# Performance work log

Hardware: AMD Instinct MI355X
Metric: run time of the kernel (lower is better)

The kernel has to match this reference:

```python
import jax, jax.numpy as jnp
import numpy as np

DIM = 128
N = 4096


def setup_inputs() -> dict:
    key = jax.random.key(0)
    ks = jax.random.split(key, 12)
    d = DIM
    s = 0.02
    inp = jax.random.normal(ks[0], (N, 2 * d), dtype=jnp.float32)
    # H = myLinear: (2d -> 5d -> 1), tanh after each layer
    Hw1 = jax.random.normal(ks[1], (2 * d, 5 * d), dtype=jnp.float32) * s
    Hb1 = jax.random.normal(ks[2], (5 * d,), dtype=jnp.float32) * s
    Hw2 = jax.random.normal(ks[3], (5 * d, 1), dtype=jnp.float32) * s
    Hb2 = jax.random.normal(ks[4], (1,), dtype=jnp.float32) * s
    # augment_f: (d -> 4d -> 8d -> d*d), tanh after each layer
    Aw1 = jax.random.normal(ks[5], (d, 4 * d), dtype=jnp.float32) * s
    Ab1 = jax.random.normal(ks[6], (4 * d,), dtype=jnp.float32) * s
    Aw2 = jax.random.normal(ks[7], (4 * d, 8 * d), dtype=jnp.float32) * s
    Ab2 = jax.random.normal(ks[8], (8 * d,), dtype=jnp.float32) * s
    Aw3 = jax.random.normal(ks[9], (8 * d, d * d), dtype=jnp.float32) * s
    Ab3 = jax.random.normal(ks[10], (d * d,), dtype=jnp.float32) * s
    u = jax.random.uniform(ks[11], (d,), dtype=jnp.float32, minval=-0.001, maxval=0.001)
    return {"t": 0, "inp": inp, "Hw1": Hw1, "Hb1": Hb1, "Hw2": Hw2, "Hb2": Hb2,
            "Aw1": Aw1, "Ab1": Ab1, "Aw2": Aw2, "Ab2": Ab2, "Aw3": Aw3, "Ab3": Ab3, "u": u}


def reference(t, inp, Hw1, Hb1, Hw2, Hb2, Aw1, Ab1, Aw2, Ab2, Aw3, Ab3, u):
    d = DIM
    n = inp.shape[0]

    def H_scalar(z):  # z: [2d] -> scalar
        h = jnp.tanh(z @ Hw1 + Hb1)
        return jnp.tanh(h @ Hw2 + Hb2)[0]

    # per-sample gradient of scalar H w.r.t. input (== batch_jacobian squeeze)
    g = jax.vmap(jax.grad(H_scalar))(inp)  # [N, 2d]
    dx = g[:, :d]
    dv = -g[:, d:]

    x = inp[:, :d]
    h1 = jnp.tanh(x @ Aw1 + Ab1)            # [N, 4d]
    h2 = jnp.tanh(h1 @ Aw2 + Ab2)           # [N, 8d]
    gq = jnp.tanh(h2 @ Aw3 + Ab3).reshape(n, d, d)  # [N, d, d]
    dv = dv + jnp.einsum("nij,j->ni", gq, u)
    return jnp.concatenate([dx, dv], axis=-1)  # [N, 2d]
```

## Files before the change

kernel.cpp:

```cpp
#include <hip/hip_runtime.h>
#include <hip/hip_bf16.h>
#include <cstdint>


typedef __bf16 bf16_t;
typedef __bf16 bf16x4_t __attribute__((ext_vector_type(4)));
typedef __bf16 bf16x8_t __attribute__((ext_vector_type(8)));
typedef float f32x4_t __attribute__((ext_vector_type(4)));
typedef float f32x16_t __attribute__((ext_vector_type(16)));
typedef int intx4_t __attribute__((ext_vector_type(4)));
typedef int intx8_t __attribute__((ext_vector_type(8)));

#define DIMD 128
#define NROW 4096
#define SMEM_G64 8192
#define SMEM3_BYTES 73728

__device__ __forceinline__ float fast_tanh(float x) {
  float t = __builtin_amdgcn_exp2f(x * 2.8853900817779268f);
  return 1.f - 2.f * __builtin_amdgcn_rcpf(t + 1.f);
}

__device__ __forceinline__ uint8_t to_fp8(float x) {
  return (uint8_t)(__builtin_amdgcn_cvt_pk_fp8_f32(x, x, 0, false) & 0xff);
}

__device__ __forceinline__ void g2l16(const void* gp, void* lp) {
  __builtin_amdgcn_global_load_lds(
      reinterpret_cast<__attribute__((address_space(1))) void*>(
          reinterpret_cast<uintptr_t>(gp)),
      reinterpret_cast<__attribute__((address_space(3))) void*>(
          reinterpret_cast<uintptr_t>(lp)),
      16, 0, 0);
}

template <int CTRL>
__device__ __forceinline__ float dpp_addf(float v) {
  return v + __int_as_float(__builtin_amdgcn_update_dpp(
                 0, __float_as_int(v), CTRL, 0xf, 0xf, true));
}
__device__ __forceinline__ float dpp_sum32(float v) {
  v = dpp_addf<0x111>(v);
  v = dpp_addf<0x112>(v);
  v = dpp_addf<0x114>(v);
  v = dpp_addf<0x118>(v);
  v = dpp_addf<0x142>(v);
  return v;
}

template <int EPI>
__device__ __forceinline__ void gemm64_body(char* smem, int bx, int by,
                                            const bf16_t* A, int lda,
                                            const bf16_t* B, int ldb, int K,
                                            const float* bias, void* outp,
                                            int ldo) {
  constexpr int BK = 32;
  bf16_t* As = (bf16_t*)smem;
  bf16_t* Bs = As + 2048;

  const int m0 = bx * 64;
  const int n0 = by * 64;
  const int tid = threadIdx.x;
  const int wave = tid >> 6;
  const int lane = tid & 63;
  const int wm = wave >> 1;
  const int wn = wave & 1;

  const int sr = lane >> 2;
  const int sk = (((lane & 3) ^ ((sr >> 1) & 3)) * 8);
  const int fr = lane & 15;
  const int fk = (((lane >> 4) ^ ((fr >> 1) & 3)) * 8);

  f32x4_t acc[2][2] = {};

  for (int k0 = 0; k0 < K; k0 += BK) {
    if (k0) __syncthreads();
    const int rb = wave * 16;
    g2l16(A + (size_t)(m0 + rb + sr) * lda + (k0 + sk), As + rb * BK);
    g2l16(B + (size_t)(n0 + rb + sr) * ldb + (k0 + sk), Bs + rb * BK);
    __syncthreads();

    bf16x8_t af[2], bb[2];
#pragma unroll
    for (int t = 0; t < 2; ++t) {
      af[t] = *(const bf16x8_t*)(As + (wm * 32 + t * 16 + fr) * BK + fk);
      bb[t] = *(const bf16x8_t*)(Bs + (wn * 32 + t * 16 + fr) * BK + fk);
    }
#pragma unroll
    for (int i = 0; i < 2; ++i)
#pragma unroll
      for (int j = 0; j < 2; ++j)
        acc[i][j] = __builtin_amdgcn_mfma_f32_16x16x32_bf16(af[i], bb[j],
                                                            acc[i][j], 0, 0, 0);
  }

#pragma unroll
  for (int i = 0; i < 2; ++i) {
    const int row = m0 + wm * 32 + i * 16 + (lane >> 4) * 4;
#pragma unroll
    for (int j = 0; j < 2; ++j) {
      const int col = n0 + wn * 32 + j * 16 + fr;
      if constexpr (EPI == 0) {
        bf16_t* O = (bf16_t*)outp;
        const float b = bias[col];
#pragma unroll
        for (int r = 0; r < 4; ++r)
          O[(size_t)(row + r) * ldo + col] = (bf16_t)fast_tanh(acc[i][j][r] + b);
      } else {
        uint8_t* O = (uint8_t*)outp;
        const float b = bias[col];
#pragma unroll
        for (int r = 0; r < 4; ++r)
          O[(size_t)(row + r) * ldo + col] =
              to_fp8(64.f * fast_tanh(acc[i][j][r] + b));
      }
    }
  }
}

__device__ __forceinline__ void hbwd64_body(char* smem, int bx, int by,
                                            const bf16_t* A, int lda,
                                            const bf16_t* B, int ldb, int K,
                                            float* out, int ldo) {
  constexpr int BK = 32;
  bf16_t* As = (bf16_t*)smem;
  bf16_t* Bs = As + 2048;

  const int m0 = bx * 64;
  const int n0 = by * 64;
  const int tid = threadIdx.x;
  const int wave = tid >> 6;
  const int lane = tid & 63;
  const int wm = wave >> 2;
  const int wn = wave & 3;

  const int sr = lane >> 2;
  const int sk = (((lane & 3) ^ ((sr >> 1) & 3)) * 8);
  const int fr = lane & 15;
  const int fk = (((lane >> 4) ^ ((fr >> 1) & 3)) * 8);

  f32x4_t acc[2] = {};

  for (int k0 = 0; k0 < K; k0 += BK) {
    if (k0) __syncthreads();
    if (wave < 4) {
      const int rb = wave * 16;
      g2l16(A + (size_t)(m0 + rb + sr) * lda + (k0 + sk), As + rb * BK);
    } else {
      const int rb = (wave - 4) * 16;
      g2l16(B + (size_t)(n0 + rb + sr) * ldb + (k0 + sk), Bs + rb * BK);
    }
    __syncthreads();

    const bf16x8_t bb = *(const bf16x8_t*)(Bs + (wn * 16 + fr) * BK + fk);
#pragma unroll
    for (int t = 0; t < 2; ++t) {
      const bf16x8_t af =
          *(const bf16x8_t*)(As + (wm * 32 + t * 16 + fr) * BK + fk);
      acc[t] = __builtin_amdgcn_mfma_f32_16x16x32_bf16(af, bb, acc[t], 0, 0, 0);
    }
  }

  const bool dx = (n0 < DIMD);
  const int col = n0 + wn * 16 + fr;
#pragma unroll
  for (int t = 0; t < 2; ++t) {
    const int row = m0 + wm * 32 + t * 16 + (lane >> 4) * 4;
#pragma unroll
    for (int r = 0; r < 4; ++r) {
      const size_t idx = (size_t)(row + r) * ldo + col;
      if (dx) out[idx] = acc[t][r];
      else atomicAdd(&out[idx], -acc[t][r]);
    }
  }
}

__device__ __forceinline__ void a3_body(char* smem, int bx, int by,
                                        const uint8_t* A, const uint8_t* B,
                                        float* out, const float* ab3,
                                        const float* uvec) {
  constexpr int BK = 64, K = 1024, NT = K / BK;
  uint8_t* As = (uint8_t*)smem;
  uint8_t* Bs = As + 49152;

  const int m0 = bx * 256;
  const int n0 = by * 128;
  const int tid = threadIdx.x;
  const int wave = tid >> 6;
  const int lane = tid & 63;
  const int wm = wave >> 1;
  const int wn = wave & 1;

  const int sr = lane >> 2;
  const int sk = ((lane & 3) ^ ((sr >> 1) & 3)) * 16;

  const int rl = lane & 31;
  const int w = (rl >> 1) & 3;
  const int c0 = lane >> 5;
  const int sLo = ((2 * c0) ^ w) * 16;
  const int sHi = ((2 * c0 + 1) ^ w) * 16;

  f32x16_t acc[2][2] = {};

#define A3_STAGE(buf, k0)                                                     \
  do {                                                                        \
    uint8_t* Ad = As + (buf) * 16384;                                         \
    uint8_t* Bd = Bs + (buf) * 8192;                                          \
    _Pragma("unroll") for (int t_ = 0; t_ < 2; ++t_) {                        \
      const int rb_ = wave * 32 + t_ * 16;                                    \
      g2l16(A + (size_t)(m0 + rb_ + sr) * K + ((k0) + sk), Ad + rb_ * BK);    \
    }                                                                         \
    const int rbB_ = wave * 16;                                               \
    g2l16(B + (size_t)(n0 + rbB_ + sr) * K + ((k0) + sk), Bd + rbB_ * BK);    \
  } while (0)

  A3_STAGE(0, 0);
  A3_STAGE(1, BK);
  asm volatile("s_waitcnt vmcnt(3)" ::: "memory");
  __builtin_amdgcn_s_barrier();
  asm volatile("" ::: "memory");

  int cur = 0, pre = 2;
#pragma unroll 1
  for (int t = 0; t < NT; ++t) {
    if (t + 2 < NT) A3_STAGE(pre, (t + 2) * BK);
    const uint8_t* Ab = As + cur * 16384;
    const uint8_t* Bb = Bs + cur * 8192;

    __builtin_amdgcn_s_setprio(1);
    intx8_t bfr[2];
#pragma unroll
    for (int j = 0; j < 2; ++j) {
      const int rb2 = (wn * 64 + j * 32 + rl) * BK;
      intx4_t lob = *(const intx4_t*)(Bb + rb2 + sLo);
      intx4_t hib = *(const intx4_t*)(Bb + rb2 + sHi);
      bfr[j] = __builtin_shufflevector(lob, hib, 0, 1, 2, 3, 4, 5, 6, 7);
    }
#pragma unroll
    for (int i = 0; i < 2; ++i) {
      const int ra = (wm * 64 + i * 32 + rl) * BK;
      intx4_t lo = *(const intx4_t*)(Ab + ra + sLo);
      intx4_t hi = *(const intx4_t*)(Ab + ra + sHi);
      intx8_t af = __builtin_shufflevector(lo, hi, 0, 1, 2, 3, 4, 5, 6, 7);
#pragma unroll
      for (int j = 0; j < 2; ++j)
        acc[i][j] = __builtin_amdgcn_mfma_scale_f32_32x32x64_f8f6f4(
            af, bfr[j], acc[i][j], 0, 0, 0, 0x79797979, 0, 0x79797979);
    }
    __builtin_amdgcn_s_setprio(0);

    if (t < NT - 1) {
      if (t + 2 < NT)
        asm volatile("s_waitcnt vmcnt(3)" ::: "memory");
      else
        asm volatile("s_waitcnt vmcnt(0)" ::: "memory");
      __builtin_amdgcn_s_barrier();
      asm volatile("" ::: "memory");
    }
    cur = (cur == 2) ? 0 : cur + 1;
    pre = (pre == 2) ? 0 : pre + 1;
  }
#undef A3_STAGE

  const int q = lane >> 5;
  const int cA = wn * 64 + rl;
  const float uu0 = uvec[cA];
  const float uu1 = uvec[cA + 32];
  const float b30 = ab3[n0 + cA];
  const float b31 = ab3[n0 + cA + 32];
#pragma unroll
  for (int i = 0; i < 2; ++i) {
    float s16[16];
#pragma unroll
    for (int r = 0; r < 16; ++r)
      s16[r] = fast_tanh(acc[i][0][r] + b30) * uu0 +
               fast_tanh(acc[i][1][r] + b31) * uu1;
#pragma unroll
    for (int r = 0; r < 16; ++r) s16[r] = dpp_sum32(s16[r]);
    if (rl == 31) {
      const int rowb = m0 + wm * 64 + i * 32 + 4 * q;
#pragma unroll
      for (int r = 0; r < 16; ++r)
        atomicAdd(
            &out[(size_t)(rowb + (r & 3) + 8 * (r >> 2)) * 256 + 128 + by],
            s16[r]);
    }
  }
}

__device__ __forceinline__ void tcvt_body(char* smem, const float* in,
                                          bf16_t* out, int R, int C, int bx,
                                          int by) {
  float(*t)[33] = (float(*)[33])smem;
  const int c0 = bx * 32;
  const int r0 = by * 32;
  const int tx = threadIdx.x & 31;
  const int ty = threadIdx.x >> 5;
#pragma unroll
  for (int k = 0; k < 4; ++k)
    t[ty + k * 8][tx] = in[(size_t)(r0 + ty + k * 8) * C + c0 + tx];
  __syncthreads();
#pragma unroll
  for (int k = 0; k < 4; ++k)
    out[(size_t)(c0 + ty + k * 8) * R + r0 + tx] = (bf16_t)t[tx][ty + k * 8];
}

__device__ __forceinline__ void aw3t_body(char* smem, const float* Aw3,
                                          uint8_t* Aw3T8, int b) {
  float(*t)[33] = (float(*)[33])smem;
  const int c0 = (b & 511) * 32;
  const int r0 = (b >> 9) * 32;
  const int tx = threadIdx.x & 31;
  const int ty = threadIdx.x >> 5;
#pragma unroll
  for (int k = 0; k < 4; ++k)
    t[ty + k * 8][tx] = Aw3[(size_t)(r0 + ty + k * 8) * 16384 + c0 + tx];
  __syncthreads();
  const int cl = threadIdx.x >> 3;
  const int j = (threadIdx.x & 7) * 4;
  uchar4 v;
  v.x = to_fp8(64.f * t[j + 0][cl]);
  v.y = to_fp8(64.f * t[j + 1][cl]);
  v.z = to_fp8(64.f * t[j + 2][cl]);
  v.w = to_fp8(64.f * t[j + 3][cl]);
  *(uchar4*)(Aw3T8 + (size_t)(c0 + cl) * 1024 + r0 + j) = v;
}

__device__ __forceinline__ void hgrad_row(int row, const bf16_t* h,
                                          const float* Hw2, const float* Hb2,
                                          bf16_t* wout) {
  const int lane = threadIdx.x & 63;
  float hv[10], wv[10];
  float pre2 = 0.f;
#pragma unroll
  for (int t = 0; t < 10; ++t) {
    const int j = lane + t * 64;
    hv[t] = (float)h[(size_t)row * 640 + j];
    wv[t] = Hw2[j];
    pre2 += hv[t] * wv[t];
  }
#pragma unroll
  for (int d = 1; d < 64; d <<= 1) pre2 += __shfl_xor(pre2, d, 64);
  const float y = fast_tanh(pre2 + Hb2[0]);
  const float s = 1.f - y * y;
#pragma unroll
  for (int t = 0; t < 10; ++t) {
    const int j = lane + t * 64;
    wout[(size_t)row * 640 + j] = (bf16_t)(s * wv[t] * (1.f - hv[t] * hv[t]));
  }
}

__global__ __launch_bounds__(256) void launch0(
    const float* __restrict__ inp, bf16_t* __restrict__ inp_bf,
    const float* __restrict__ Hw1, bf16_t* __restrict__ Hw1T,
    bf16_t* __restrict__ Hw1_bf, const float* __restrict__ Aw1,
    bf16_t* __restrict__ Aw1T, const float* __restrict__ Aw2,
    bf16_t* __restrict__ Aw2T, float* __restrict__ out) {
  __shared__ __align__(16) char smem[4224];
  int b = blockIdx.x;
  if (b < 1024) {
    const int i = b * 256 + threadIdx.x;
    const float4 v = ((const float4*)inp)[i];
    bf16x4_t o = {(bf16_t)v.x, (bf16_t)v.y, (bf16_t)v.z, (bf16_t)v.w};
    ((bf16x4_t*)inp_bf)[i] = o;
  } else if (b < 1184) {
    int s = b - 1024;
    tcvt_body(smem, Hw1, Hw1T, 256, 640, s % 20, s / 20);
  } else if (b < 1248) {
    int s = b - 1184;
    tcvt_body(smem, Aw1, Aw1T, 128, 512, s % 16, s / 16);
  } else if (b < 1760) {
    int s = b - 1248;
    tcvt_body(smem, Aw2, Aw2T, 512, 1024, s % 32, s / 32);
  } else if (b < 1920) {
    const int i = (b - 1760) * 256 + threadIdx.x;
    const float4 v = ((const float4*)Hw1)[i];
    bf16x4_t o = {(bf16_t)v.x, (bf16_t)v.y, (bf16_t)v.z, (bf16_t)v.w};
    ((bf16x4_t*)Hw1_bf)[i] = o;
  } else {
    const int i = (b - 1920) * 256 + threadIdx.x;
    ((float4*)out)[i] = make_float4(0.f, 0.f, 0.f, 0.f);
  }
}

__global__ __launch_bounds__(256) void launch1(
    const bf16_t* __restrict__ inp_bf, const bf16_t* __restrict__ Hw1T,
    const float* __restrict__ Hb1, bf16_t* __restrict__ h_bf,
    const bf16_t* __restrict__ Aw1T, const float* __restrict__ Ab1,
    bf16_t* __restrict__ h1_bf, const float* __restrict__ Aw3,
    uint8_t* __restrict__ Aw3T8) {
  __shared__ __align__(16) char smem[SMEM_G64];
  const int b = blockIdx.x;
  if (b < 640) {
    gemm64_body<0>(smem, b % 64, b / 64, inp_bf, 256, Hw1T, 256, 256, Hb1,
                   h_bf, 640);
  } else if (b < 1152) {
    const int i = b - 640;
    gemm64_body<0>(smem, i % 64, i / 64, inp_bf, 256, Aw1T, 128, 128, Ab1,
                   h1_bf, 512);
  } else {
    aw3t_body(smem, Aw3, Aw3T8, b - 1152);
  }
}

__global__ __launch_bounds__(256) void launch2(
    const bf16_t* __restrict__ h1_bf, const bf16_t* __restrict__ Aw2T,
    const float* __restrict__ Ab2, uint8_t* __restrict__ h2_f8,
    const bf16_t* __restrict__ h_bf, const float* __restrict__ Hw2,
    const float* __restrict__ Hb2, bf16_t* __restrict__ w_bf,
    const float* __restrict__ Aw3, uint8_t* __restrict__ Aw3T8) {
  __shared__ __align__(16) char smem[SMEM_G64];
  const int b = blockIdx.x;
  if (b < 1024) {
    gemm64_body<3>(smem, b % 64, b / 64, h1_bf, 512, Aw2T, 512, 512, Ab2,
                   h2_f8, 1024);
  } else if (b < 2048) {
    const int row = (b - 1024) * 4 + (threadIdx.x >> 6);
    hgrad_row(row, h_bf, Hw2, Hb2, w_bf);
  } else {
    aw3t_body(smem, Aw3, Aw3T8, 8192 + (b - 2048));
  }
}

__global__ __launch_bounds__(512, 4) void launch3(
    const bf16_t* __restrict__ w_bf, const bf16_t* __restrict__ Hw1_bf,
    float* __restrict__ out, const uint8_t* __restrict__ h2_f8,
    const uint8_t* __restrict__ Aw3T8, const float* __restrict__ Ab3,
    const float* __restrict__ uvec) {
  __shared__ __align__(16) char smem[SMEM3_BYTES];
  const int b = blockIdx.x;
  if (b < 256) {
    hbwd64_body(smem, b % 64, b / 64, w_bf, 640, Hw1_bf, 640, 640, out, 256);
  } else {
    const int p = b - 256;
    const int by = (p & 7) * 16 + ((p >> 3) & 15);
    const int bx = p >> 7;
    a3_body(smem, bx, by, h2_f8, Aw3T8, out, Ab3, uvec);
  }
}

extern "C" void kernel_launch(void* const* d_in, const int* in_sizes, int n_in,
                              void* d_out, int out_size, void* d_ws,
                              size_t ws_size, hipStream_t stream) {
  (void)in_sizes; (void)n_in; (void)out_size; (void)ws_size;
  const float* inp = (const float*)d_in[1];
  const float* Hw1 = (const float*)d_in[2];
  const float* Hb1 = (const float*)d_in[3];
  const float* Hw2 = (const float*)d_in[4];
  const float* Hb2 = (const float*)d_in[5];
  const float* Aw1 = (const float*)d_in[6];
  const float* Ab1 = (const float*)d_in[7];
  const float* Aw2 = (const float*)d_in[8];
  const float* Ab2 = (const float*)d_in[9];
  const float* Aw3 = (const float*)d_in[10];
  const float* Ab3 = (const float*)d_in[11];
  const float* u = (const float*)d_in[12];
  float* out = (float*)d_out;

  char* ws = (char*)d_ws;
  bf16_t* inp_bf = (bf16_t*)ws;   ws += (size_t)NROW * 256 * 2;
  bf16_t* Hw1_bf = (bf16_t*)ws;   ws += (size_t)256 * 640 * 2;
  bf16_t* Hw1T = (bf16_t*)ws;     ws += (size_t)640 * 256 * 2;
  bf16_t* Aw1T = (bf16_t*)ws;     ws += (size_t)512 * 128 * 2;
  bf16_t* Aw2T = (bf16_t*)ws;     ws += (size_t)1024 * 512 * 2;
  uint8_t* Aw3T8 = (uint8_t*)ws;  ws += (size_t)16384 * 1024;
  bf16_t* h_bf = (bf16_t*)ws;     ws += (size_t)NROW * 640 * 2;
  bf16_t* w_bf = (bf16_t*)ws;     ws += (size_t)NROW * 640 * 2;
  bf16_t* h1_bf = (bf16_t*)ws;    ws += (size_t)NROW * 512 * 2;
  uint8_t* h2_f8 = (uint8_t*)ws;  ws += (size_t)NROW * 1024;

  launch0<<<2944, 256, 0, stream>>>(inp, inp_bf, Hw1, Hw1T, Hw1_bf, Aw1, Aw1T,
                                    Aw2, Aw2T, out);
  launch1<<<9344, 256, 0, stream>>>(inp_bf, Hw1T, Hb1, h_bf, Aw1T, Ab1, h1_bf,
                                    Aw3, Aw3T8);
  launch2<<<10240, 256, 0, stream>>>(h1_bf, Aw2T, Ab2, h2_f8, h_bf, Hw2, Hb2,
                                     w_bf, Aw3, Aw3T8);
  launch3<<<2304, 512, 0, stream>>>(w_bf, Hw1_bf, out, h2_f8, Aw3T8, Ab3, u);
}
```

Before: 238.1 us.

## Triple-buffer GEMM LDS staging and widen Aw3 fp8 transpose tiles

The 64x64 GEMM and H-backward bodies now use a three-stage LDS ring with async global-to-LDS loads issued two tiles ahead. A single barrier per iteration, gated by explicit vmcnt waits, replaces the paired syncthreads, so global load latency overlaps MFMA work. The Aw3 transpose-and-fp8-quantize step now handles 128x128 tiles with float4 loads and packed 4-byte fp8 conversion, which cuts its block count and narrow memory accesses. In exchange, shared memory per block rises, which may lower occupancy in launch1 and launch2.

```diff
diff --git a/kernel.cpp b/kernel.cpp
--- a/kernel.cpp
+++ b/kernel.cpp
@@ -13,7 +13,7 @@
 
 #define DIMD 128
 #define NROW 4096
-#define SMEM_G64 8192
+#define SMEM_G64 24576
 #define SMEM3_BYTES 73728
 
 __device__ __forceinline__ float fast_tanh(float x) {
@@ -23,6 +23,12 @@
 
 __device__ __forceinline__ uint8_t to_fp8(float x) {
   return (uint8_t)(__builtin_amdgcn_cvt_pk_fp8_f32(x, x, 0, false) & 0xff);
+}
+
+__device__ __forceinline__ uint32_t pk4_fp8(float a, float b, float c,
+                                            float d) {
+  uint32_t lo = (uint32_t)__builtin_amdgcn_cvt_pk_fp8_f32(a, b, 0, false);
+  return (uint32_t)__builtin_amdgcn_cvt_pk_fp8_f32(c, d, lo, true);
 }
 
 __device__ __forceinline__ void g2l16(const void* gp, void* lp) {
@@ -56,7 +62,8 @@
                                             int ldo) {
   constexpr int BK = 32;
   bf16_t* As = (bf16_t*)smem;
-  bf16_t* Bs = As + 2048;
+  bf16_t* Bs = As + 3 * 2048;
+  const int NT = K / BK;
 
   const int m0 = bx * 64;
   const int n0 = by * 64;
@@ -70,21 +77,35 @@
   const int sk = (((lane & 3) ^ ((sr >> 1) & 3)) * 8);
   const int fr = lane & 15;
   const int fk = (((lane >> 4) ^ ((fr >> 1) & 3)) * 8);
+  const int rb = wave * 16;
+
+  const bf16_t* Ag = A + (size_t)(m0 + rb + sr) * lda + sk;
+  const bf16_t* Bg = B + (size_t)(n0 + rb + sr) * ldb + sk;
+
+#define G64_STAGE(buf, k0)                              \
+  do {                                                  \
+    g2l16(Ag + (k0), As + (buf) * 2048 + rb * BK);      \
+    g2l16(Bg + (k0), Bs + (buf) * 2048 + rb * BK);      \
+  } while (0)
 
   f32x4_t acc[2][2] = {};
 
-  for (int k0 = 0; k0 < K; k0 += BK) {
-    if (k0) __syncthreads();
-    const int rb = wave * 16;
-    g2l16(A + (size_t)(m0 + rb + sr) * lda + (k0 + sk), As + rb * BK);
-    g2l16(B + (size_t)(n0 + rb + sr) * ldb + (k0 + sk), Bs + rb * BK);
-    __syncthreads();
+  G64_STAGE(0, 0);
+  G64_STAGE(1, BK);
+  asm volatile("s_waitcnt vmcnt(2)" ::: "memory");
+  __builtin_amdgcn_s_barrier();
+  asm volatile("" ::: "memory");
+
+  for (int t = 0; t < NT; ++t) {
+    if (t + 2 < NT) G64_STAGE((t + 2) % 3, (t + 2) * BK);
+    const bf16_t* Ab = As + (t % 3) * 2048;
+    const bf16_t* Bb = Bs + (t % 3) * 2048;
 
     bf16x8_t af[2], bb[2];
 #pragma unroll
-    for (int t = 0; t < 2; ++t) {
-      af[t] = *(const bf16x8_t*)(As + (wm * 32 + t * 16 + fr) * BK + fk);
-      bb[t] = *(const bf16x8_t*)(Bs + (wn * 32 + t * 16 + fr) * BK + fk);
+    for (int u = 0; u < 2; ++u) {
+      af[u] = *(const bf16x8_t*)(Ab + (wm * 32 + u * 16 + fr) * BK + fk);
+      bb[u] = *(const bf16x8_t*)(Bb + (wn * 32 + u * 16 + fr) * BK + fk);
     }
 #pragma unroll
     for (int i = 0; i < 2; ++i)
@@ -92,7 +113,16 @@
       for (int j = 0; j < 2; ++j)
         acc[i][j] = __builtin_amdgcn_mfma_f32_16x16x32_bf16(af[i], bb[j],
                                                             acc[i][j], 0, 0, 0);
-  }
+    if (t < NT - 1) {
+      if (t + 2 < NT)
+        asm volatile("s_waitcnt vmcnt(2)" ::: "memory");
+      else
+        asm volatile("s_waitcnt vmcnt(0)" ::: "memory");
+      __builtin_amdgcn_s_barrier();
+      asm volatile("" ::: "memory");
+    }
+  }
+#undef G64_STAGE
 
 #pragma unroll
   for (int i = 0; i < 2; ++i) {
@@ -124,7 +154,8 @@
                                             float* out, int ldo) {
   constexpr int BK = 32;
   bf16_t* As = (bf16_t*)smem;
-  bf16_t* Bs = As + 2048;
+  bf16_t* Bs = As + 3 * 2048;
+  const int NT = K / BK;
 
   const int m0 = bx * 64;
   const int n0 = by * 64;
@@ -139,25 +170,38 @@
   const int fr = lane & 15;
   const int fk = (((lane >> 4) ^ ((fr >> 1) & 3)) * 8);
 
+  const int rbs = (wave & 3) * 16;
+  const bf16_t* Sg = (wave < 4) ? A + (size_t)(m0 + rbs + sr) * lda + sk
+                                : B + (size_t)(n0 + rbs + sr) * ldb + sk;
+  bf16_t* Sl = ((wave < 4) ? As : Bs) + rbs * BK;
+
   f32x4_t acc[2] = {};
 
-  for (int k0 = 0; k0 < K; k0 += BK) {
-    if (k0) __syncthreads();
-    if (wave < 4) {
-      const int rb = wave * 16;
-      g2l16(A + (size_t)(m0 + rb + sr) * lda + (k0 + sk), As + rb * BK);
-    } else {
-      const int rb = (wave - 4) * 16;
-      g2l16(B + (size_t)(n0 + rb + sr) * ldb + (k0 + sk), Bs + rb * BK);
-    }
-    __syncthreads();
-
-    const bf16x8_t bb = *(const bf16x8_t*)(Bs + (wn * 16 + fr) * BK + fk);
-#pragma unroll
-    for (int t = 0; t < 2; ++t) {
+  g2l16(Sg, Sl);
+  g2l16(Sg + BK, Sl + 2048);
+  asm volatile("s_waitcnt vmcnt(1)" ::: "memory");
+  __builtin_amdgcn_s_barrier();
+  asm volatile("" ::: "memory");
+
+  for (int t = 0; t < NT; ++t) {
+    if (t + 2 < NT) g2l16(Sg + (t + 2) * BK, Sl + ((t + 2) % 3) * 2048);
+    const bf16_t* Ab = As + (t % 3) * 2048;
+    const bf16_t* Bb = Bs + (t % 3) * 2048;
+
+    const bf16x8_t bb = *(const bf16x8_t*)(Bb + (wn * 16 + fr) * BK + fk);
+#pragma unroll
+    for (int u = 0; u < 2; ++u) {
       const bf16x8_t af =
-          *(const bf16x8_t*)(As + (wm * 32 + t * 16 + fr) * BK + fk);
-      acc[t] = __builtin_amdgcn_mfma_f32_16x16x32_bf16(af, bb, acc[t], 0, 0, 0);
+          *(const bf16x8_t*)(Ab + (wm * 32 + u * 16 + fr) * BK + fk);
+      acc[u] = __builtin_amdgcn_mfma_f32_16x16x32_bf16(af, bb, acc[u], 0, 0, 0);
+    }
+    if (t < NT - 1) {
+      if (t + 2 < NT)
+        asm volatile("s_waitcnt vmcnt(1)" ::: "memory");
+      else
+        asm volatile("s_waitcnt vmcnt(0)" ::: "memory");
+      __builtin_amdgcn_s_barrier();
+      asm volatile("" ::: "memory");
     }
   }
 
@@ -307,23 +351,32 @@
 
 __device__ __forceinline__ void aw3t_body(char* smem, const float* Aw3,
                                           uint8_t* Aw3T8, int b) {
-  float(*t)[33] = (float(*)[33])smem;
-  const int c0 = (b & 511) * 32;
-  const int r0 = (b >> 9) * 32;
+  uint32_t(*T)[33] = (uint32_t(*)[33])smem;
+  const int ct = b & 127;
+  const int rt = b >> 7;
+  const size_t c0 = (size_t)ct * 128;
+  const int r0 = rt * 128;
   const int tx = threadIdx.x & 31;
-  const int ty = threadIdx.x >> 5;
-#pragma unroll
-  for (int k = 0; k < 4; ++k)
-    t[ty + k * 8][tx] = Aw3[(size_t)(r0 + ty + k * 8) * 16384 + c0 + tx];
+  const int g = threadIdx.x >> 5;
+#pragma unroll
+  for (int k = 0; k < 4; ++k) {
+    const int rr = r0 + 4 * g + 32 * k;
+    const float4 v0 = *(const float4*)(Aw3 + (size_t)(rr + 0) * 16384 + c0 + 4 * tx);
+    const float4 v1 = *(const float4*)(Aw3 + (size_t)(rr + 1) * 16384 + c0 + 4 * tx);
+    const float4 v2 = *(const float4*)(Aw3 + (size_t)(rr + 2) * 16384 + c0 + 4 * tx);
+    const float4 v3 = *(const float4*)(Aw3 + (size_t)(rr + 3) * 16384 + c0 + 4 * tx);
+    const int r4 = g + 8 * k;
+    T[4 * tx + 0][r4] = pk4_fp8(64.f * v0.x, 64.f * v1.x, 64.f * v2.x, 64.f * v3.x);
+    T[4 * tx + 1][r4] = pk4_fp8(64.f * v0.y, 64.f * v1.y, 64.f * v2.y, 64.f * v3.y);
+    T[4 * tx + 2][r4] = pk4_fp8(64.f * v0.z, 64.f * v1.z, 64.f * v2.z, 64.f * v3.z);
+    T[4 * tx + 3][r4] = pk4_fp8(64.f * v0.w, 64.f * v1.w, 64.f * v2.w, 64.f * v3.w);
+  }
   __syncthreads();
-  const int cl = threadIdx.x >> 3;
-  const int j = (threadIdx.x & 7) * 4;
-  uchar4 v;
-  v.x = to_fp8(64.f * t[j + 0][cl]);
-  v.y = to_fp8(64.f * t[j + 1][cl]);
-  v.z = to_fp8(64.f * t[j + 2][cl]);
-  v.w = to_fp8(64.f * t[j + 3][cl]);
-  *(uchar4*)(Aw3T8 + (size_t)(c0 + cl) * 1024 + r0 + j) = v;
+#pragma unroll
+  for (int k2 = 0; k2 < 16; ++k2) {
+    const int cc = g + 8 * k2;
+    *(uint32_t*)(Aw3T8 + (c0 + cc) * 1024 + r0 + 4 * tx) = T[cc][tx];
+  }
 }
 
 __device__ __forceinline__ void hgrad_row(int row, const bf16_t* h,
@@ -418,7 +471,7 @@
     const int row = (b - 1024) * 4 + (threadIdx.x >> 6);
     hgrad_row(row, h_bf, Hw2, Hb2, w_bf);
   } else {
-    aw3t_body(smem, Aw3, Aw3T8, 8192 + (b - 2048));
+    aw3t_body(smem, Aw3, Aw3T8, 512 + (b - 2048));
   }
 }
 
@@ -471,9 +524,9 @@
 
   launch0<<<2944, 256, 0, stream>>>(inp, inp_bf, Hw1, Hw1T, Hw1_bf, Aw1, Aw1T,
                                     Aw2, Aw2T, out);
-  launch1<<<9344, 256, 0, stream>>>(inp_bf, Hw1T, Hb1, h_bf, Aw1T, Ab1, h1_bf,
+  launch1<<<1664, 256, 0, stream>>>(inp_bf, Hw1T, Hb1, h_bf, Aw1T, Ab1, h1_bf,
                                     Aw3, Aw3T8);
-  launch2<<<10240, 256, 0, stream>>>(h1_bf, Aw2T, Ab2, h2_f8, h_bf, Hw2, Hb2,
-                                     w_bf, Aw3, Aw3T8);
+  launch2<<<2560, 256, 0, stream>>>(h1_bf, Aw2T, Ab2, h2_f8, h_bf, Hw2, Hb2,
+                                    w_bf, Aw3, Aw3T8);
   launch3<<<2304, 512, 0, stream>>>(w_bf, Hw1_bf, out, h2_f8, Aw3T8, Ab3, u);
 }
```

Measured after the change: 238.7 us. Within noise of the previous version (+0.2%).
